# Optimization experiments

Hardware: AMD Instinct MI355X
Metric: run time of the kernel (lower is better)

The kernel has to match this reference:

```python
import jax, jax.numpy as jnp
import numpy as np

B, S, D = 2, 2048, 1024
E, K = 8, 2
I = 938  # expert intermediate: _find_multiple(round(4*1024*2/3),256)//3 = 2816//3


def setup_inputs() -> dict:
    key = jax.random.key(0)
    ks = jax.random.split(key, 6)
    inv_sqrt_d = 1.0 / np.sqrt(D)
    inv_sqrt_i = 1.0 / np.sqrt(I)
    return {
        "hidden_states": jax.random.normal(ks[0], (B, S, D), jnp.float32),
        "gate_weight": jax.random.normal(ks[1], (E, D), jnp.float32) * inv_sqrt_d,
        "shared_gate_up": jax.random.normal(ks[2], (D, 2 * I), jnp.float32) * inv_sqrt_d,
        "shared_down": jax.random.normal(ks[3], (I, D), jnp.float32) * inv_sqrt_i,
        "expert_gate_up": jax.random.normal(ks[4], (E, D, 2 * I), jnp.float32) * inv_sqrt_d,
        "expert_down": jax.random.normal(ks[5], (E, I, D), jnp.float32) * inv_sqrt_i,
    }


def _swiglu(gu, w_down):
    gate, up = jnp.split(gu, 2, axis=-1)
    return (jax.nn.silu(gate) * up) @ w_down


def reference(hidden_states, gate_weight, shared_gate_up, shared_down,
              expert_gate_up, expert_down):
    b, s, d = hidden_states.shape
    x = hidden_states.reshape(-1, d)            # [T, D]
    T = x.shape[0]
    n_experts = gate_weight.shape[0]

    # shared expert (always active)
    out = _swiglu(x @ shared_gate_up, shared_down)

    # router: softmax in fp32, top-k, renormalize
    logits = x @ gate_weight.T                   # [T, E]
    probs = jax.nn.softmax(logits.astype(jnp.float32), axis=-1).astype(x.dtype)
    top_p, top_i = jax.lax.top_k(probs, K)       # [T, K]
    top_p = top_p / (top_p.sum(axis=-1, keepdims=True) + 1e-8)

    # dense combine weights: combine[t, e] = sum_k top_p[t,k] * [top_i[t,k]==e]
    combine = jnp.zeros((T, n_experts), x.dtype).at[
        jnp.arange(T)[:, None], top_i].add(top_p)

    # same math as per-token gathered bmm: sum_e combine[:,e] * expert_e(x)
    for e in range(n_experts):
        out = out + combine[:, e:e + 1] * _swiglu(x @ expert_gate_up[e], expert_down[e])

    return out.reshape(b, s, d)
```

## Files before the change

### kernel.cpp

```cpp
#include <hip/hip_runtime.h>
#include <hip/hip_bf16.h>
#include <stdint.h>

#define T_TOK 4096
#define D_DIM 1024
#define E_EXP 8
#define I_DIM 938
#define TWO_I 1876
#define NP2 2048
#define IP 1024

typedef __attribute__((ext_vector_type(8))) short bf16x8;
typedef __attribute__((ext_vector_type(4))) float f32x4;
typedef __attribute__((ext_vector_type(8))) unsigned short u16x8;
typedef __attribute__((ext_vector_type(4))) unsigned short u16x4;

static __device__ __forceinline__ unsigned short f2bf(float f) {
  union { float f; uint32_t u; } v; v.f = f;
  uint32_t r = v.u + 0x7fffu + ((v.u >> 16) & 1u);
  return (unsigned short)(r >> 16);
}
static __device__ __forceinline__ void gload16(const void* g, void* l) {
  __builtin_amdgcn_global_load_lds((__attribute__((address_space(1))) void*)g,
                                   (__attribute__((address_space(3))) void*)l, 16, 0, 0);
}

__global__ __launch_bounds__(256) void cvt_x_kernel(const float* __restrict__ x,
                                                    unsigned short* __restrict__ xb) {
  int i = blockIdx.x * 256 + threadIdx.x;
  float4 v = reinterpret_cast<const float4*>(x)[i];
  u16x4 o;
  o[0] = f2bf(v.x); o[1] = f2bf(v.y); o[2] = f2bf(v.z); o[3] = f2bf(v.w);
  reinterpret_cast<u16x4*>(xb)[i] = o;
}

__global__ __launch_bounds__(256) void router_kernel(const float* __restrict__ x,
                                                     const float* __restrict__ gw,
                                                     int* __restrict__ ti,
                                                     float* __restrict__ tw) {
  int t = blockIdx.x * 4 + (threadIdx.x >> 6);
  int lane = threadIdx.x & 63;
  const float* xp = x + (size_t)t * D_DIM;
  float xv[16];
  #pragma unroll
  for (int i = 0; i < 16; ++i) xv[i] = xp[lane + i * 64];
  float logit[E_EXP];
  #pragma unroll
  for (int e = 0; e < E_EXP; ++e) {
    const float* wp = gw + (size_t)e * D_DIM;
    float s = 0.f;
    #pragma unroll
    for (int i = 0; i < 16; ++i) s += xv[i] * wp[lane + i * 64];
    #pragma unroll
    for (int o = 32; o; o >>= 1) s += __shfl_xor(s, o);
    logit[e] = s;
  }
  float mx = logit[0];
  #pragma unroll
  for (int e = 1; e < E_EXP; ++e) mx = fmaxf(mx, logit[e]);
  float p[E_EXP], sum = 0.f;
  #pragma unroll
  for (int e = 0; e < E_EXP; ++e) { p[e] = __expf(logit[e] - mx); sum += p[e]; }
  int i1 = 0; float p1 = p[0];
  #pragma unroll
  for (int e = 1; e < E_EXP; ++e) if (p[e] > p1) { p1 = p[e]; i1 = e; }
  int i2 = -1; float p2 = -1.f;
  #pragma unroll
  for (int e = 0; e < E_EXP; ++e) if (e != i1 && p[e] > p2) { p2 = p[e]; i2 = e; }
  float P1 = p1 / sum, P2 = p2 / sum;
  float denom = P1 + P2 + 1e-8f;
  if (lane == 0) {
    ti[2 * t] = i1; ti[2 * t + 1] = i2;
    tw[2 * t] = P1 / denom; tw[2 * t + 1] = P2 / denom;
  }
}

__global__ void zero_cnt_kernel(int* cnt) { if (threadIdx.x < E_EXP) cnt[threadIdx.x] = 0; }

__global__ __launch_bounds__(256) void assign_kernel(const int* __restrict__ ti,
                                                     const float* __restrict__ tw,
                                                     int* __restrict__ cnt,
                                                     int* __restrict__ list,
                                                     float* __restrict__ wl, int cap) {
  int t = blockIdx.x * 256 + threadIdx.x;
  #pragma unroll
  for (int j = 0; j < 2; ++j) {
    int e = ti[2 * t + j];
    float w = tw[2 * t + j];
    int slot = atomicAdd(&cnt[e], 1);
    if (slot < cap) { list[e * cap + slot] = t; wl[e * cap + slot] = w; }
  }
}

__global__ __launch_bounds__(256) void transpose_gu_kernel(
    const float* __restrict__ sgu, const float* __restrict__ egu,
    unsigned short* __restrict__ wT) {
  int e = blockIdx.z;
  const float* w = (e == 0) ? sgu : egu + (size_t)(e - 1) * D_DIM * TWO_I;
  unsigned short* o = wT + (size_t)e * NP2 * D_DIM;
  int k0 = blockIdx.x * 64, n0 = blockIdx.y * 32;
  __shared__ unsigned short lds[32][72];
  int tid = threadIdx.x;
  int nn = tid & 31, kr = tid >> 5;
  int n = n0 + nn;
  int src = (n < IP) ? ((n < I_DIM) ? n : -1)
                     : ((n - IP < I_DIM) ? I_DIM + (n - IP) : -1);
  #pragma unroll
  for (int i = 0; i < 8; ++i) {
    int k = k0 + kr + i * 8;
    float f = (src >= 0) ? w[(size_t)k * TWO_I + src] : 0.f;
    lds[nn][kr + i * 8] = f2bf(f);
  }
  __syncthreads();
  int nr = tid >> 3, kc = (tid & 7) * 8;
  u16x8 v;
  #pragma unroll
  for (int j = 0; j < 8; ++j) v[j] = lds[nr][kc + j];
  *reinterpret_cast<u16x8*>(&o[(size_t)(n0 + nr) * D_DIM + k0 + kc]) = v;
}

__global__ __launch_bounds__(256) void transpose_d_kernel(
    const float* __restrict__ sdn, const float* __restrict__ edn,
    unsigned short* __restrict__ wT) {
  int e = blockIdx.z;
  const float* w = (e == 0) ? sdn : edn + (size_t)(e - 1) * I_DIM * D_DIM;
  unsigned short* o = wT + (size_t)e * D_DIM * IP;
  int k0 = blockIdx.x * 64, n0 = blockIdx.y * 32;
  __shared__ unsigned short lds[32][72];
  int tid = threadIdx.x;
  int nn = tid & 31, kr = tid >> 5;
  #pragma unroll
  for (int i = 0; i < 8; ++i) {
    int k = k0 + kr + i * 8;
    float f = (k < I_DIM) ? w[(size_t)k * D_DIM + n0 + nn] : 0.f;
    lds[nn][kr + i * 8] = f2bf(f);
  }
  __syncthreads();
  int nr = tid >> 3, kc = (tid & 7) * 8;
  u16x8 v;
  #pragma unroll
  for (int j = 0; j < 8; ++j) v[j] = lds[nr][kc + j];
  *reinterpret_cast<u16x8*>(&o[(size_t)(n0 + nr) * IP + k0 + kc]) = v;
}

template<bool GATHER>
__global__ __launch_bounds__(256) void gemm1_kernel(
    const unsigned short* __restrict__ xb,
    const unsigned short* __restrict__ wbase,
    unsigned short* __restrict__ hbase,
    const int* __restrict__ list, const int* __restrict__ cnt, int cap) {
  const int e = blockIdx.z;
  const int m0 = blockIdx.x * 128, n0 = blockIdx.y * 128;
  int count = T_TOK;
  if (GATHER) { count = min(cnt[e], cap); if (m0 >= count) return; }
  const unsigned short* w = wbase + (GATHER ? (size_t)(e + 1) * NP2 * D_DIM : 0);
  unsigned short* h = hbase + (GATHER ? (size_t)e * cap * IP : 0);

  __shared__ __align__(16) unsigned short a_lds[128 * 32];
  __shared__ __align__(16) unsigned short b_lds[256 * 32];
  const int tid = threadIdx.x;
  const int wave = tid >> 6, lane = tid & 63;
  const int mw = (wave >> 1) * 64, nw = (wave & 1) * 64;
  const int fr = lane & 15, fq = lane >> 4;

  const int ko = (tid & 3) * 8;
  int arow[2];
  #pragma unroll
  for (int r = 0; r < 2; ++r) {
    int lr = (tid >> 2) + 64 * r;
    int trow = m0 + lr;
    if (GATHER) trow = list[e * cap + min(trow, count - 1)];
    arow[r] = trow;
  }
  size_t brow[4];
  #pragma unroll
  for (int r = 0; r < 4; ++r) {
    int lr = (tid >> 2) + 64 * r;
    int grow = (lr < 128) ? (n0 + lr) : (IP + n0 + lr - 128);
    brow[r] = (size_t)grow * D_DIM;
  }

  f32x4 accg[4][4], accu[4][4];
  #pragma unroll
  for (int m = 0; m < 4; ++m)
    #pragma unroll
    for (int n = 0; n < 4; ++n) { accg[m][n] = (f32x4)0.f; accu[m][n] = (f32x4)0.f; }

  for (int k0 = 0; k0 < D_DIM; k0 += 32) {
    __syncthreads();
    #pragma unroll
    for (int r = 0; r < 2; ++r)
      gload16(xb + (size_t)arow[r] * D_DIM + k0 + ko, &a_lds[((tid >> 2) + 64 * r) * 32 + ko]);
    #pragma unroll
    for (int r = 0; r < 4; ++r)
      gload16(w + brow[r] + k0 + ko, &b_lds[((tid >> 2) + 64 * r) * 32 + ko]);
    __syncthreads();
    bf16x8 av[4], bg[4], bu[4];
    #pragma unroll
    for (int m = 0; m < 4; ++m)
      av[m] = *reinterpret_cast<const bf16x8*>(&a_lds[(mw + m * 16 + fr) * 32 + fq * 8]);
    #pragma unroll
    for (int n = 0; n < 4; ++n) {
      bg[n] = *reinterpret_cast<const bf16x8*>(&b_lds[(nw + n * 16 + fr) * 32 + fq * 8]);
      bu[n] = *reinterpret_cast<const bf16x8*>(&b_lds[(128 + nw + n * 16 + fr) * 32 + fq * 8]);
    }
    #pragma unroll
    for (int m = 0; m < 4; ++m)
      #pragma unroll
      for (int n = 0; n < 4; ++n) {
        accg[m][n] = __builtin_amdgcn_mfma_f32_16x16x32_bf16(av[m], bg[n], accg[m][n], 0, 0, 0);
        accu[m][n] = __builtin_amdgcn_mfma_f32_16x16x32_bf16(av[m], bu[n], accu[m][n], 0, 0, 0);
      }
  }
  #pragma unroll
  for (int m = 0; m < 4; ++m)
    #pragma unroll
    for (int q = 0; q < 4; ++q) {
      int t = m0 + mw + m * 16 + fq * 4 + q;
      #pragma unroll
      for (int n = 0; n < 4; ++n) {
        float g = accg[m][n][q], u = accu[m][n][q];
        float hv = (g / (1.f + __expf(-g))) * u;
        h[(size_t)t * IP + n0 + nw + n * 16 + fr] = f2bf(hv);
      }
    }
}

template<bool GATHER>
__global__ __launch_bounds__(256) void gemm2_kernel(
    const unsigned short* __restrict__ hbase,
    const unsigned short* __restrict__ wbase,
    float* __restrict__ out,
    const int* __restrict__ list, const float* __restrict__ wl,
    const int* __restrict__ cnt, int cap) {
  const int e = blockIdx.z;
  const int m0 = blockIdx.x * 128, n0 = blockIdx.y * 128;
  int count = T_TOK;
  if (GATHER) { count = min(cnt[e], cap); if (m0 >= count) return; }
  const unsigned short* A = hbase + (GATHER ? (size_t)e * cap * IP : 0);
  const unsigned short* B = wbase + (GATHER ? (size_t)(e + 1) * D_DIM * IP : 0);

  __shared__ __align__(16) unsigned short a_lds[128 * 32];
  __shared__ __align__(16) unsigned short b_lds[128 * 32];
  const int tid = threadIdx.x;
  const int wave = tid >> 6, lane = tid & 63;
  const int mw = (wave >> 1) * 64, nw = (wave & 1) * 64;
  const int fr = lane & 15, fq = lane >> 4;
  const int ko = (tid & 3) * 8;

  f32x4 acc[4][4];
  #pragma unroll
  for (int m = 0; m < 4; ++m)
    #pragma unroll
    for (int n = 0; n < 4; ++n) acc[m][n] = (f32x4)0.f;

  for (int k0 = 0; k0 < IP; k0 += 32) {
    __syncthreads();
    #pragma unroll
    for (int r = 0; r < 2; ++r) {
      int lr = (tid >> 2) + 64 * r;
      gload16(A + (size_t)(m0 + lr) * IP + k0 + ko, &a_lds[lr * 32 + ko]);
      gload16(B + (size_t)(n0 + lr) * IP + k0 + ko, &b_lds[lr * 32 + ko]);
    }
    __syncthreads();
    bf16x8 av[4], bv[4];
    #pragma unroll
    for (int m = 0; m < 4; ++m)
      av[m] = *reinterpret_cast<const bf16x8*>(&a_lds[(mw + m * 16 + fr) * 32 + fq * 8]);
    #pragma unroll
    for (int n = 0; n < 4; ++n)
      bv[n] = *reinterpret_cast<const bf16x8*>(&b_lds[(nw + n * 16 + fr) * 32 + fq * 8]);
    #pragma unroll
    for (int m = 0; m < 4; ++m)
      #pragma unroll
      for (int n = 0; n < 4; ++n)
        acc[m][n] = __builtin_amdgcn_mfma_f32_16x16x32_bf16(av[m], bv[n], acc[m][n], 0, 0, 0);
  }
  #pragma unroll
  for (int m = 0; m < 4; ++m)
    #pragma unroll
    for (int q = 0; q < 4; ++q) {
      int slot = m0 + mw + m * 16 + fq * 4 + q;
      if (GATHER) {
        if (slot < count) {
          int t = list[e * cap + slot];
          float wgt = wl[e * cap + slot];
          #pragma unroll
          for (int n = 0; n < 4; ++n)
            atomicAdd(&out[(size_t)t * D_DIM + n0 + nw + n * 16 + fr], wgt * acc[m][n][q]);
        }
      } else {
        #pragma unroll
        for (int n = 0; n < 4; ++n)
          out[(size_t)slot * D_DIM + n0 + nw + n * 16 + fr] = acc[m][n][q];
      }
    }
}

extern "C" void kernel_launch(void* const* d_in, const int* in_sizes, int n_in,
                              void* d_out, int out_size, void* d_ws, size_t ws_size,
                              hipStream_t stream) {
  const float* x   = (const float*)d_in[0];
  const float* gw  = (const float*)d_in[1];
  const float* sgu = (const float*)d_in[2];
  const float* sdn = (const float*)d_in[3];
  const float* egu = (const float*)d_in[4];
  const float* edn = (const float*)d_in[5];
  float* out = (float*)d_out;

  char* p = (char*)d_ws;
  unsigned short* xb = (unsigned short*)p;  p += (size_t)T_TOK * D_DIM * 2;
  unsigned short* wTgu = (unsigned short*)p; p += (size_t)9 * NP2 * D_DIM * 2;
  unsigned short* wTd  = (unsigned short*)p; p += (size_t)9 * D_DIM * IP * 2;
  size_t fixed_tail = (size_t)T_TOK * 2 * (4 + 4) + 64 + 256;
  size_t used = (size_t)(p - (char*)d_ws) + fixed_tail;
  size_t per_cap = (size_t)E_EXP * (IP * 2 + 4 + 4);
  long avail = (long)ws_size - (long)used;
  int cap = (int)(avail > 0 ? avail / (long)per_cap : 0);
  cap &= ~127;
  if (cap > 2048) cap = 2048;
  if (cap < 1280) cap = 1280;
  if ((size_t)E_EXP * cap * IP < (size_t)T_TOK * IP) cap = 1280;

  unsigned short* h_g = (unsigned short*)p; p += (size_t)E_EXP * cap * IP * 2;
  int*   ti   = (int*)p;   p += (size_t)T_TOK * 2 * 4;
  float* tw   = (float*)p; p += (size_t)T_TOK * 2 * 4;
  int*   list = (int*)p;   p += (size_t)E_EXP * cap * 4;
  float* wl   = (float*)p; p += (size_t)E_EXP * cap * 4;
  int*   cnt  = (int*)p;

  cvt_x_kernel<<<(T_TOK * D_DIM) / (4 * 256), 256, 0, stream>>>(x, xb);
  router_kernel<<<T_TOK / 4, 256, 0, stream>>>(x, gw, ti, tw);
  zero_cnt_kernel<<<1, 64, 0, stream>>>(cnt);
  assign_kernel<<<T_TOK / 256, 256, 0, stream>>>(ti, tw, cnt, list, wl, cap);
  transpose_gu_kernel<<<dim3(D_DIM / 64, NP2 / 32, 9), 256, 0, stream>>>(sgu, egu, wTgu);
  transpose_d_kernel<<<dim3(IP / 64, D_DIM / 32, 9), 256, 0, stream>>>(sdn, edn, wTd);

  gemm1_kernel<false><<<dim3(T_TOK / 128, IP / 128, 1), 256, 0, stream>>>(
      xb, wTgu, h_g, nullptr, nullptr, cap);
  gemm2_kernel<false><<<dim3(T_TOK / 128, D_DIM / 128, 1), 256, 0, stream>>>(
      h_g, wTd, out, nullptr, nullptr, nullptr, cap);
  gemm1_kernel<true><<<dim3(cap / 128, IP / 128, E_EXP), 256, 0, stream>>>(
      xb, wTgu, h_g, list, cnt, cap);
  gemm2_kernel<true><<<dim3(cap / 128, D_DIM / 128, E_EXP), 256, 0, stream>>>(
      h_g, wTd, out, list, wl, cnt, cap);
}
```

Measured before the change: 481.1 us.

## Double-buffer GEMM LDS tiles, merge shared/routed gemm1 launch, remap blocks across XCDs

The GEMM main loops now use two LDS buffers. The next k-tile's global-to-LDS loads are issued before the current tile's MFMAs, with one barrier per iteration instead of two, so load latency can overlap compute. The shared-expert and routed-expert gate/up GEMMs run in a single flattened launch, and the shared expert writes to its own intermediate buffer. Block indices are remapped so that consecutive tiles spread across the chiplet groups. The cost is double the LDS per block, which can lower occupancy, and the routed grids are now sized for a fixed capacity rather than the computed cap.

```diff
diff --git a/kernel.cpp b/kernel.cpp
--- a/kernel.cpp
+++ b/kernel.cpp
@@ -143,39 +143,47 @@
   *reinterpret_cast<u16x8*>(&o[(size_t)(n0 + nr) * IP + k0 + kc]) = v;
 }
 
-template<bool GATHER>
 __global__ __launch_bounds__(256) void gemm1_kernel(
     const unsigned short* __restrict__ xb,
-    const unsigned short* __restrict__ wbase,
-    unsigned short* __restrict__ hbase,
+    const unsigned short* __restrict__ wTgu,
+    unsigned short* __restrict__ h_sh,
+    unsigned short* __restrict__ h_g,
     const int* __restrict__ list, const int* __restrict__ cnt, int cap) {
-  const int e = blockIdx.z;
-  const int m0 = blockIdx.x * 128, n0 = blockIdx.y * 128;
+  const int orig = blockIdx.x;
+  const int wg = (orig & 7) * (gridDim.x >> 3) + (orig >> 3);
+  const int e = wg >> 8;
+  const int rem = wg & 255;
+  const int m0 = (rem >> 3) * 128, n0 = (rem & 7) * 128;
   int count = T_TOK;
-  if (GATHER) { count = min(cnt[e], cap); if (m0 >= count) return; }
-  const unsigned short* w = wbase + (GATHER ? (size_t)(e + 1) * NP2 * D_DIM : 0);
-  unsigned short* h = hbase + (GATHER ? (size_t)e * cap * IP : 0);
-
-  __shared__ __align__(16) unsigned short a_lds[128 * 32];
-  __shared__ __align__(16) unsigned short b_lds[256 * 32];
+  const unsigned short* w = wTgu;
+  unsigned short* h = h_sh;
+  if (e > 0) {
+    count = min(cnt[e - 1], cap);
+    if (m0 >= count) return;
+    w = wTgu + (size_t)e * NP2 * D_DIM;
+    h = h_g + (size_t)(e - 1) * cap * IP;
+  }
+
+  __shared__ __align__(16) unsigned short a_lds[2][128 * 32];
+  __shared__ __align__(16) unsigned short b_lds[2][256 * 32];
   const int tid = threadIdx.x;
   const int wave = tid >> 6, lane = tid & 63;
   const int mw = (wave >> 1) * 64, nw = (wave & 1) * 64;
   const int fr = lane & 15, fq = lane >> 4;
-
   const int ko = (tid & 3) * 8;
-  int arow[2];
+  const int ldr = tid >> 2;
+
+  size_t arow[2];
   #pragma unroll
   for (int r = 0; r < 2; ++r) {
-    int lr = (tid >> 2) + 64 * r;
-    int trow = m0 + lr;
-    if (GATHER) trow = list[e * cap + min(trow, count - 1)];
-    arow[r] = trow;
+    int trow = m0 + ldr + 64 * r;
+    if (e > 0) trow = list[(e - 1) * cap + min(trow, count - 1)];
+    arow[r] = (size_t)trow * D_DIM;
   }
   size_t brow[4];
   #pragma unroll
   for (int r = 0; r < 4; ++r) {
-    int lr = (tid >> 2) + 64 * r;
+    int lr = ldr + 64 * r;
     int grow = (lr < 128) ? (n0 + lr) : (IP + n0 + lr - 128);
     brow[r] = (size_t)grow * D_DIM;
   }
@@ -186,23 +194,28 @@
     #pragma unroll
     for (int n = 0; n < 4; ++n) { accg[m][n] = (f32x4)0.f; accu[m][n] = (f32x4)0.f; }
 
-  for (int k0 = 0; k0 < D_DIM; k0 += 32) {
-    __syncthreads();
+  auto stage = [&](int buf, int k0) {
     #pragma unroll
     for (int r = 0; r < 2; ++r)
-      gload16(xb + (size_t)arow[r] * D_DIM + k0 + ko, &a_lds[((tid >> 2) + 64 * r) * 32 + ko]);
+      gload16(xb + arow[r] + k0 + ko, &a_lds[buf][(ldr + 64 * r) * 32 + ko]);
     #pragma unroll
     for (int r = 0; r < 4; ++r)
-      gload16(w + brow[r] + k0 + ko, &b_lds[((tid >> 2) + 64 * r) * 32 + ko]);
-    __syncthreads();
+      gload16(w + brow[r] + k0 + ko, &b_lds[buf][(ldr + 64 * r) * 32 + ko]);
+  };
+
+  stage(0, 0);
+  __syncthreads();
+  int cur = 0;
+  for (int t = 0; t < D_DIM / 32; ++t) {
+    if (t + 1 < D_DIM / 32) stage(cur ^ 1, (t + 1) * 32);
     bf16x8 av[4], bg[4], bu[4];
     #pragma unroll
     for (int m = 0; m < 4; ++m)
-      av[m] = *reinterpret_cast<const bf16x8*>(&a_lds[(mw + m * 16 + fr) * 32 + fq * 8]);
+      av[m] = *reinterpret_cast<const bf16x8*>(&a_lds[cur][(mw + m * 16 + fr) * 32 + fq * 8]);
     #pragma unroll
     for (int n = 0; n < 4; ++n) {
-      bg[n] = *reinterpret_cast<const bf16x8*>(&b_lds[(nw + n * 16 + fr) * 32 + fq * 8]);
-      bu[n] = *reinterpret_cast<const bf16x8*>(&b_lds[(128 + nw + n * 16 + fr) * 32 + fq * 8]);
+      bg[n] = *reinterpret_cast<const bf16x8*>(&b_lds[cur][(nw + n * 16 + fr) * 32 + fq * 8]);
+      bu[n] = *reinterpret_cast<const bf16x8*>(&b_lds[cur][(128 + nw + n * 16 + fr) * 32 + fq * 8]);
     }
     #pragma unroll
     for (int m = 0; m < 4; ++m)
@@ -211,6 +224,8 @@
         accg[m][n] = __builtin_amdgcn_mfma_f32_16x16x32_bf16(av[m], bg[n], accg[m][n], 0, 0, 0);
         accu[m][n] = __builtin_amdgcn_mfma_f32_16x16x32_bf16(av[m], bu[n], accu[m][n], 0, 0, 0);
       }
+    __syncthreads();
+    cur ^= 1;
   }
   #pragma unroll
   for (int m = 0; m < 4; ++m)
@@ -226,27 +241,19 @@
     }
 }
 
-template<bool GATHER>
-__global__ __launch_bounds__(256) void gemm2_kernel(
-    const unsigned short* __restrict__ hbase,
-    const unsigned short* __restrict__ wbase,
-    float* __restrict__ out,
-    const int* __restrict__ list, const float* __restrict__ wl,
-    const int* __restrict__ cnt, int cap) {
-  const int e = blockIdx.z;
+__global__ __launch_bounds__(256) void gemm2_sh_kernel(
+    const unsigned short* __restrict__ A,
+    const unsigned short* __restrict__ B,
+    float* __restrict__ out) {
   const int m0 = blockIdx.x * 128, n0 = blockIdx.y * 128;
-  int count = T_TOK;
-  if (GATHER) { count = min(cnt[e], cap); if (m0 >= count) return; }
-  const unsigned short* A = hbase + (GATHER ? (size_t)e * cap * IP : 0);
-  const unsigned short* B = wbase + (GATHER ? (size_t)(e + 1) * D_DIM * IP : 0);
-
-  __shared__ __align__(16) unsigned short a_lds[128 * 32];
-  __shared__ __align__(16) unsigned short b_lds[128 * 32];
+  __shared__ __align__(16) unsigned short a_lds[2][128 * 32];
+  __shared__ __align__(16) unsigned short b_lds[2][128 * 32];
   const int tid = threadIdx.x;
   const int wave = tid >> 6, lane = tid & 63;
   const int mw = (wave >> 1) * 64, nw = (wave & 1) * 64;
   const int fr = lane & 15, fq = lane >> 4;
   const int ko = (tid & 3) * 8;
+  const int ldr = tid >> 2;
 
   f32x4 acc[4][4];
   #pragma unroll
@@ -254,45 +261,115 @@
     #pragma unroll
     for (int n = 0; n < 4; ++n) acc[m][n] = (f32x4)0.f;
 
-  for (int k0 = 0; k0 < IP; k0 += 32) {
-    __syncthreads();
+  auto stage = [&](int buf, int k0) {
     #pragma unroll
     for (int r = 0; r < 2; ++r) {
-      int lr = (tid >> 2) + 64 * r;
-      gload16(A + (size_t)(m0 + lr) * IP + k0 + ko, &a_lds[lr * 32 + ko]);
-      gload16(B + (size_t)(n0 + lr) * IP + k0 + ko, &b_lds[lr * 32 + ko]);
-    }
-    __syncthreads();
+      int lr = ldr + 64 * r;
+      gload16(A + (size_t)(m0 + lr) * IP + k0 + ko, &a_lds[buf][lr * 32 + ko]);
+      gload16(B + (size_t)(n0 + lr) * IP + k0 + ko, &b_lds[buf][lr * 32 + ko]);
+    }
+  };
+  stage(0, 0);
+  __syncthreads();
+  int cur = 0;
+  for (int t = 0; t < IP / 32; ++t) {
+    if (t + 1 < IP / 32) stage(cur ^ 1, (t + 1) * 32);
     bf16x8 av[4], bv[4];
     #pragma unroll
     for (int m = 0; m < 4; ++m)
-      av[m] = *reinterpret_cast<const bf16x8*>(&a_lds[(mw + m * 16 + fr) * 32 + fq * 8]);
+      av[m] = *reinterpret_cast<const bf16x8*>(&a_lds[cur][(mw + m * 16 + fr) * 32 + fq * 8]);
     #pragma unroll
     for (int n = 0; n < 4; ++n)
-      bv[n] = *reinterpret_cast<const bf16x8*>(&b_lds[(nw + n * 16 + fr) * 32 + fq * 8]);
+      bv[n] = *reinterpret_cast<const bf16x8*>(&b_lds[cur][(nw + n * 16 + fr) * 32 + fq * 8]);
     #pragma unroll
     for (int m = 0; m < 4; ++m)
       #pragma unroll
       for (int n = 0; n < 4; ++n)
         acc[m][n] = __builtin_amdgcn_mfma_f32_16x16x32_bf16(av[m], bv[n], acc[m][n], 0, 0, 0);
+    __syncthreads();
+    cur ^= 1;
+  }
+  #pragma unroll
+  for (int m = 0; m < 4; ++m)
+    #pragma unroll
+    for (int q = 0; q < 4; ++q) {
+      int t = m0 + mw + m * 16 + fq * 4 + q;
+      #pragma unroll
+      for (int n = 0; n < 4; ++n)
+        out[(size_t)t * D_DIM + n0 + nw + n * 16 + fr] = acc[m][n][q];
+    }
+}
+
+__global__ __launch_bounds__(256) void gemm2_rt_kernel(
+    const unsigned short* __restrict__ h_g,
+    const unsigned short* __restrict__ wTd,
+    float* __restrict__ out,
+    const int* __restrict__ list, const float* __restrict__ wl,
+    const int* __restrict__ cnt, int cap) {
+  const int orig = blockIdx.x;
+  const int wg = (orig & 7) * (gridDim.x >> 3) + (orig >> 3);
+  const int e = wg >> 7;
+  const int rem = wg & 127;
+  const int m0 = (rem >> 3) * 128, n0 = (rem & 7) * 128;
+  const int count = min(cnt[e], cap);
+  if (m0 >= count) return;
+  const unsigned short* A = h_g + (size_t)e * cap * IP;
+  const unsigned short* B = wTd + (size_t)(e + 1) * D_DIM * IP;
+
+  __shared__ __align__(16) unsigned short a_lds[2][128 * 32];
+  __shared__ __align__(16) unsigned short b_lds[2][128 * 32];
+  const int tid = threadIdx.x;
+  const int wave = tid >> 6, lane = tid & 63;
+  const int mw = (wave >> 1) * 64, nw = (wave & 1) * 64;
+  const int fr = lane & 15, fq = lane >> 4;
+  const int ko = (tid & 3) * 8;
+  const int ldr = tid >> 2;
+
+  f32x4 acc[4][4];
+  #pragma unroll
+  for (int m = 0; m < 4; ++m)
+    #pragma unroll
+    for (int n = 0; n < 4; ++n) acc[m][n] = (f32x4)0.f;
+
+  auto stage = [&](int buf, int k0) {
+    #pragma unroll
+    for (int r = 0; r < 2; ++r) {
+      int lr = ldr + 64 * r;
+      gload16(A + (size_t)(m0 + lr) * IP + k0 + ko, &a_lds[buf][lr * 32 + ko]);
+      gload16(B + (size_t)(n0 + lr) * IP + k0 + ko, &b_lds[buf][lr * 32 + ko]);
+    }
+  };
+  stage(0, 0);
+  __syncthreads();
+  int cur = 0;
+  for (int t = 0; t < IP / 32; ++t) {
+    if (t + 1 < IP / 32) stage(cur ^ 1, (t + 1) * 32);
+    bf16x8 av[4], bv[4];
+    #pragma unroll
+    for (int m = 0; m < 4; ++m)
+      av[m] = *reinterpret_cast<const bf16x8*>(&a_lds[cur][(mw + m * 16 + fr) * 32 + fq * 8]);
+    #pragma unroll
+    for (int n = 0; n < 4; ++n)
+      bv[n] = *reinterpret_cast<const bf16x8*>(&b_lds[cur][(nw + n * 16 + fr) * 32 + fq * 8]);
+    #pragma unroll
+    for (int m = 0; m < 4; ++m)
+      #pragma unroll
+      for (int n = 0; n < 4; ++n)
+        acc[m][n] = __builtin_amdgcn_mfma_f32_16x16x32_bf16(av[m], bv[n], acc[m][n], 0, 0, 0);
+    __syncthreads();
+    cur ^= 1;
   }
   #pragma unroll
   for (int m = 0; m < 4; ++m)
     #pragma unroll
     for (int q = 0; q < 4; ++q) {
       int slot = m0 + mw + m * 16 + fq * 4 + q;
-      if (GATHER) {
-        if (slot < count) {
-          int t = list[e * cap + slot];
-          float wgt = wl[e * cap + slot];
-          #pragma unroll
-          for (int n = 0; n < 4; ++n)
-            atomicAdd(&out[(size_t)t * D_DIM + n0 + nw + n * 16 + fr], wgt * acc[m][n][q]);
-        }
-      } else {
+      if (slot < count) {
+        int t = list[e * cap + slot];
+        float wgt = wl[e * cap + slot];
         #pragma unroll
         for (int n = 0; n < 4; ++n)
-          out[(size_t)slot * D_DIM + n0 + nw + n * 16 + fr] = acc[m][n][q];
+          atomicAdd(&out[(size_t)t * D_DIM + n0 + nw + n * 16 + fr], wgt * acc[m][n][q]);
       }
     }
 }
@@ -309,9 +386,11 @@
   float* out = (float*)d_out;
 
   char* p = (char*)d_ws;
-  unsigned short* xb = (unsigned short*)p;  p += (size_t)T_TOK * D_DIM * 2;
+  unsigned short* xb   = (unsigned short*)p; p += (size_t)T_TOK * D_DIM * 2;
   unsigned short* wTgu = (unsigned short*)p; p += (size_t)9 * NP2 * D_DIM * 2;
   unsigned short* wTd  = (unsigned short*)p; p += (size_t)9 * D_DIM * IP * 2;
+  unsigned short* h_sh = (unsigned short*)p; p += (size_t)T_TOK * IP * 2;
+
   size_t fixed_tail = (size_t)T_TOK * 2 * (4 + 4) + 64 + 256;
   size_t used = (size_t)(p - (char*)d_ws) + fixed_tail;
   size_t per_cap = (size_t)E_EXP * (IP * 2 + 4 + 4);
@@ -320,7 +399,6 @@
   cap &= ~127;
   if (cap > 2048) cap = 2048;
   if (cap < 1280) cap = 1280;
-  if ((size_t)E_EXP * cap * IP < (size_t)T_TOK * IP) cap = 1280;
 
   unsigned short* h_g = (unsigned short*)p; p += (size_t)E_EXP * cap * IP * 2;
   int*   ti   = (int*)p;   p += (size_t)T_TOK * 2 * 4;
@@ -336,12 +414,7 @@
   transpose_gu_kernel<<<dim3(D_DIM / 64, NP2 / 32, 9), 256, 0, stream>>>(sgu, egu, wTgu);
   transpose_d_kernel<<<dim3(IP / 64, D_DIM / 32, 9), 256, 0, stream>>>(sdn, edn, wTd);
 
-  gemm1_kernel<false><<<dim3(T_TOK / 128, IP / 128, 1), 256, 0, stream>>>(
-      xb, wTgu, h_g, nullptr, nullptr, cap);
-  gemm2_kernel<false><<<dim3(T_TOK / 128, D_DIM / 128, 1), 256, 0, stream>>>(
-      h_g, wTd, out, nullptr, nullptr, nullptr, cap);
-  gemm1_kernel<true><<<dim3(cap / 128, IP / 128, E_EXP), 256, 0, stream>>>(
-      xb, wTgu, h_g, list, cnt, cap);
-  gemm2_kernel<true><<<dim3(cap / 128, D_DIM / 128, E_EXP), 256, 0, stream>>>(
-      h_g, wTd, out, list, wl, cnt, cap);
-}
+  gemm1_kernel<<<9 * 32 * 8, 256, 0, stream>>>(xb, wTgu, h_sh, h_g, list, cnt, cap);
+  gemm2_sh_kernel<<<dim3(T_TOK / 128, D_DIM / 128), 256, 0, stream>>>(h_sh, wTd, out);
+  gemm2_rt_kernel<<<8 * 16 * 8, 256, 0, stream>>>(h_g, wTd, out, list, wl, cnt, cap);
+}
```

Measured after the change: 489.1 us. Within noise of the previous version (+1.7%).

## Merge shared and routed expert GEMMs into single launches with 256x256 tiles

Applied to the files above, without the earlier changes.

Interleaves gate and up columns in the transposed gate_up weights so one accumulator tile holds both, and pairs them with a lane shuffle in the epilogue. GEMM tiles grow to 256x256 with K=64 per stage and 512 threads. The shared and routed expert work for each GEMM now runs in one launch with an XCD-aware block remap, and output is zeroed with a memset so the shared expert also accumulates atomically. This cuts launches and raises data reuse per tile, at the cost of higher register and LDS pressure, lower occupancy, and extra atomic traffic for the shared expert output.

```diff
diff --git a/kernel.cpp b/kernel.cpp
--- a/kernel.cpp
+++ b/kernel.cpp
@@ -103,8 +103,8 @@
   int tid = threadIdx.x;
   int nn = tid & 31, kr = tid >> 5;
   int n = n0 + nn;
-  int src = (n < IP) ? ((n < I_DIM) ? n : -1)
-                     : ((n - IP < I_DIM) ? I_DIM + (n - IP) : -1);
+  int hc = n >> 1;
+  int src = (hc < I_DIM) ? ((n & 1) ? (I_DIM + hc) : hc) : -1;
   #pragma unroll
   for (int i = 0; i < 8; ++i) {
     int k = k0 + kr + i * 8;
@@ -143,156 +143,167 @@
   *reinterpret_cast<u16x8*>(&o[(size_t)(n0 + nr) * IP + k0 + kc]) = v;
 }
 
-template<bool GATHER>
-__global__ __launch_bounds__(256) void gemm1_kernel(
+__global__ __launch_bounds__(512) void gemm1_kernel(
     const unsigned short* __restrict__ xb,
-    const unsigned short* __restrict__ wbase,
-    unsigned short* __restrict__ hbase,
+    const unsigned short* __restrict__ wTgu,
+    unsigned short* __restrict__ h_sh,
+    unsigned short* __restrict__ h_g,
     const int* __restrict__ list, const int* __restrict__ cnt, int cap) {
-  const int e = blockIdx.z;
-  const int m0 = blockIdx.x * 128, n0 = blockIdx.y * 128;
+  const int orig = blockIdx.x;
+  const int wg = (orig & 7) * (gridDim.x >> 3) + (orig >> 3);
+  int e, mb, nb;
+  if (wg < 128) { e = 0; mb = wg >> 3; nb = wg & 7; }
+  else { int r = wg - 128; e = 1 + (r >> 6); int rem = r & 63; mb = rem >> 3; nb = rem & 7; }
+  const int m0 = mb * 256, n0 = nb * 256;
   int count = T_TOK;
-  if (GATHER) { count = min(cnt[e], cap); if (m0 >= count) return; }
-  const unsigned short* w = wbase + (GATHER ? (size_t)(e + 1) * NP2 * D_DIM : 0);
-  unsigned short* h = hbase + (GATHER ? (size_t)e * cap * IP : 0);
-
-  __shared__ __align__(16) unsigned short a_lds[128 * 32];
-  __shared__ __align__(16) unsigned short b_lds[256 * 32];
+  unsigned short* h = h_sh;
+  if (e > 0) {
+    count = min(cnt[e - 1], cap);
+    if (m0 >= count) return;
+    h = h_g + (size_t)(e - 1) * cap * IP;
+  }
+  const unsigned short* w = wTgu + (size_t)e * NP2 * D_DIM;
+
+  __shared__ __align__(16) unsigned short a_lds[256 * 64];
+  __shared__ __align__(16) unsigned short b_lds[256 * 64];
   const int tid = threadIdx.x;
   const int wave = tid >> 6, lane = tid & 63;
-  const int mw = (wave >> 1) * 64, nw = (wave & 1) * 64;
+  const int mw = (wave >> 2) * 128, nw = (wave & 3) * 64;
   const int fr = lane & 15, fq = lane >> 4;
-
-  const int ko = (tid & 3) * 8;
-  int arow[2];
-  #pragma unroll
-  for (int r = 0; r < 2; ++r) {
-    int lr = (tid >> 2) + 64 * r;
-    int trow = m0 + lr;
-    if (GATHER) trow = list[e * cap + min(trow, count - 1)];
-    arow[r] = trow;
-  }
-  size_t brow[4];
-  #pragma unroll
-  for (int r = 0; r < 4; ++r) {
-    int lr = (tid >> 2) + 64 * r;
-    int grow = (lr < 128) ? (n0 + lr) : (IP + n0 + lr - 128);
-    brow[r] = (size_t)grow * D_DIM;
-  }
-
-  f32x4 accg[4][4], accu[4][4];
-  #pragma unroll
-  for (int m = 0; m < 4; ++m)
-    #pragma unroll
-    for (int n = 0; n < 4; ++n) { accg[m][n] = (f32x4)0.f; accu[m][n] = (f32x4)0.f; }
-
-  for (int k0 = 0; k0 < D_DIM; k0 += 32) {
+  const int srow = tid >> 3;
+  const int sk = (tid & 7) * 8;
+
+  size_t arow[4], brow[4];
+  #pragma unroll
+  for (int c = 0; c < 4; ++c) {
+    int rr = m0 + 64 * c + srow;
+    if (e > 0) rr = list[(e - 1) * cap + min(rr, count - 1)];
+    arow[c] = (size_t)rr * D_DIM;
+    brow[c] = (size_t)(n0 + 64 * c + srow) * D_DIM;
+  }
+
+  f32x4 acc[8][4];
+  #pragma unroll
+  for (int m = 0; m < 8; ++m)
+    #pragma unroll
+    for (int n = 0; n < 4; ++n) acc[m][n] = (f32x4)0.f;
+
+  for (int k0 = 0; k0 < D_DIM; k0 += 64) {
     __syncthreads();
     #pragma unroll
-    for (int r = 0; r < 2; ++r)
-      gload16(xb + (size_t)arow[r] * D_DIM + k0 + ko, &a_lds[((tid >> 2) + 64 * r) * 32 + ko]);
-    #pragma unroll
-    for (int r = 0; r < 4; ++r)
-      gload16(w + brow[r] + k0 + ko, &b_lds[((tid >> 2) + 64 * r) * 32 + ko]);
+    for (int c = 0; c < 4; ++c) {
+      gload16(xb + arow[c] + k0 + sk, &a_lds[(64 * c + srow) * 64 + sk]);
+      gload16(w + brow[c] + k0 + sk, &b_lds[(64 * c + srow) * 64 + sk]);
+    }
     __syncthreads();
-    bf16x8 av[4], bg[4], bu[4];
-    #pragma unroll
-    for (int m = 0; m < 4; ++m)
-      av[m] = *reinterpret_cast<const bf16x8*>(&a_lds[(mw + m * 16 + fr) * 32 + fq * 8]);
-    #pragma unroll
-    for (int n = 0; n < 4; ++n) {
-      bg[n] = *reinterpret_cast<const bf16x8*>(&b_lds[(nw + n * 16 + fr) * 32 + fq * 8]);
-      bu[n] = *reinterpret_cast<const bf16x8*>(&b_lds[(128 + nw + n * 16 + fr) * 32 + fq * 8]);
-    }
-    #pragma unroll
-    for (int m = 0; m < 4; ++m)
-      #pragma unroll
-      for (int n = 0; n < 4; ++n) {
-        accg[m][n] = __builtin_amdgcn_mfma_f32_16x16x32_bf16(av[m], bg[n], accg[m][n], 0, 0, 0);
-        accu[m][n] = __builtin_amdgcn_mfma_f32_16x16x32_bf16(av[m], bu[n], accu[m][n], 0, 0, 0);
+    #pragma unroll
+    for (int kk = 0; kk < 2; ++kk) {
+      bf16x8 av[8], bv[4];
+      #pragma unroll
+      for (int m = 0; m < 8; ++m)
+        av[m] = *reinterpret_cast<const bf16x8*>(&a_lds[(mw + m * 16 + fr) * 64 + kk * 32 + fq * 8]);
+      #pragma unroll
+      for (int n = 0; n < 4; ++n)
+        bv[n] = *reinterpret_cast<const bf16x8*>(&b_lds[(nw + n * 16 + fr) * 64 + kk * 32 + fq * 8]);
+      #pragma unroll
+      for (int m = 0; m < 8; ++m)
+        #pragma unroll
+        for (int n = 0; n < 4; ++n)
+          acc[m][n] = __builtin_amdgcn_mfma_f32_16x16x32_bf16(av[m], bv[n], acc[m][n], 0, 0, 0);
+    }
+  }
+  const bool isGate = !(fr & 1);
+  const int hcb = (n0 + nw) >> 1;
+  #pragma unroll
+  for (int m = 0; m < 8; ++m)
+    #pragma unroll
+    for (int n = 0; n < 4; ++n)
+      #pragma unroll
+      for (int q = 0; q < 4; ++q) {
+        float v = acc[m][n][q];
+        float pt = __shfl_xor(v, 1);
+        if (isGate) {
+          float hv = (v / (1.f + __expf(-v))) * pt;
+          int trow = m0 + mw + m * 16 + fq * 4 + q;
+          h[(size_t)trow * IP + hcb + n * 8 + (fr >> 1)] = f2bf(hv);
+        }
       }
-  }
-  #pragma unroll
-  for (int m = 0; m < 4; ++m)
-    #pragma unroll
-    for (int q = 0; q < 4; ++q) {
-      int t = m0 + mw + m * 16 + fq * 4 + q;
-      #pragma unroll
-      for (int n = 0; n < 4; ++n) {
-        float g = accg[m][n][q], u = accu[m][n][q];
-        float hv = (g / (1.f + __expf(-g))) * u;
-        h[(size_t)t * IP + n0 + nw + n * 16 + fr] = f2bf(hv);
-      }
-    }
-}
-
-template<bool GATHER>
-__global__ __launch_bounds__(256) void gemm2_kernel(
-    const unsigned short* __restrict__ hbase,
-    const unsigned short* __restrict__ wbase,
+}
+
+__global__ __launch_bounds__(512) void gemm2_kernel(
+    const unsigned short* __restrict__ h_sh,
+    const unsigned short* __restrict__ h_g,
+    const unsigned short* __restrict__ wTd,
     float* __restrict__ out,
     const int* __restrict__ list, const float* __restrict__ wl,
     const int* __restrict__ cnt, int cap) {
-  const int e = blockIdx.z;
-  const int m0 = blockIdx.x * 128, n0 = blockIdx.y * 128;
+  const int orig = blockIdx.x;
+  const int wg = (orig & 7) * (gridDim.x >> 3) + (orig >> 3);
+  int e, mb, nb;
+  if (wg < 64) { e = -1; mb = wg >> 2; nb = wg & 3; }
+  else { int r = wg - 64; e = r >> 5; int rem = r & 31; mb = rem >> 2; nb = rem & 3; }
+  const int m0 = mb * 256, n0 = nb * 256;
   int count = T_TOK;
-  if (GATHER) { count = min(cnt[e], cap); if (m0 >= count) return; }
-  const unsigned short* A = hbase + (GATHER ? (size_t)e * cap * IP : 0);
-  const unsigned short* B = wbase + (GATHER ? (size_t)(e + 1) * D_DIM * IP : 0);
-
-  __shared__ __align__(16) unsigned short a_lds[128 * 32];
-  __shared__ __align__(16) unsigned short b_lds[128 * 32];
+  const unsigned short* A = h_sh;
+  if (e >= 0) {
+    count = min(cnt[e], cap);
+    if (m0 >= count) return;
+    A = h_g + (size_t)e * cap * IP;
+  }
+  const unsigned short* B = wTd + (size_t)(e + 1) * D_DIM * IP;
+
+  __shared__ __align__(16) unsigned short a_lds[256 * 64];
+  __shared__ __align__(16) unsigned short b_lds[256 * 64];
   const int tid = threadIdx.x;
   const int wave = tid >> 6, lane = tid & 63;
-  const int mw = (wave >> 1) * 64, nw = (wave & 1) * 64;
+  const int mw = (wave >> 2) * 128, nw = (wave & 3) * 64;
   const int fr = lane & 15, fq = lane >> 4;
-  const int ko = (tid & 3) * 8;
-
-  f32x4 acc[4][4];
-  #pragma unroll
-  for (int m = 0; m < 4; ++m)
+  const int srow = tid >> 3;
+  const int sk = (tid & 7) * 8;
+
+  f32x4 acc[8][4];
+  #pragma unroll
+  for (int m = 0; m < 8; ++m)
     #pragma unroll
     for (int n = 0; n < 4; ++n) acc[m][n] = (f32x4)0.f;
 
-  for (int k0 = 0; k0 < IP; k0 += 32) {
+  for (int k0 = 0; k0 < IP; k0 += 64) {
     __syncthreads();
     #pragma unroll
-    for (int r = 0; r < 2; ++r) {
-      int lr = (tid >> 2) + 64 * r;
-      gload16(A + (size_t)(m0 + lr) * IP + k0 + ko, &a_lds[lr * 32 + ko]);
-      gload16(B + (size_t)(n0 + lr) * IP + k0 + ko, &b_lds[lr * 32 + ko]);
+    for (int c = 0; c < 4; ++c) {
+      gload16(A + (size_t)(m0 + 64 * c + srow) * IP + k0 + sk,
+              &a_lds[(64 * c + srow) * 64 + sk]);
+      gload16(B + (size_t)(n0 + 64 * c + srow) * IP + k0 + sk,
+              &b_lds[(64 * c + srow) * 64 + sk]);
     }
     __syncthreads();
-    bf16x8 av[4], bv[4];
-    #pragma unroll
-    for (int m = 0; m < 4; ++m)
-      av[m] = *reinterpret_cast<const bf16x8*>(&a_lds[(mw + m * 16 + fr) * 32 + fq * 8]);
-    #pragma unroll
-    for (int n = 0; n < 4; ++n)
-      bv[n] = *reinterpret_cast<const bf16x8*>(&b_lds[(nw + n * 16 + fr) * 32 + fq * 8]);
-    #pragma unroll
-    for (int m = 0; m < 4; ++m)
+    #pragma unroll
+    for (int kk = 0; kk < 2; ++kk) {
+      bf16x8 av[8], bv[4];
+      #pragma unroll
+      for (int m = 0; m < 8; ++m)
+        av[m] = *reinterpret_cast<const bf16x8*>(&a_lds[(mw + m * 16 + fr) * 64 + kk * 32 + fq * 8]);
       #pragma unroll
       for (int n = 0; n < 4; ++n)
-        acc[m][n] = __builtin_amdgcn_mfma_f32_16x16x32_bf16(av[m], bv[n], acc[m][n], 0, 0, 0);
-  }
-  #pragma unroll
-  for (int m = 0; m < 4; ++m)
+        bv[n] = *reinterpret_cast<const bf16x8*>(&b_lds[(nw + n * 16 + fr) * 64 + kk * 32 + fq * 8]);
+      #pragma unroll
+      for (int m = 0; m < 8; ++m)
+        #pragma unroll
+        for (int n = 0; n < 4; ++n)
+          acc[m][n] = __builtin_amdgcn_mfma_f32_16x16x32_bf16(av[m], bv[n], acc[m][n], 0, 0, 0);
+    }
+  }
+  #pragma unroll
+  for (int m = 0; m < 8; ++m)
     #pragma unroll
     for (int q = 0; q < 4; ++q) {
       int slot = m0 + mw + m * 16 + fq * 4 + q;
-      if (GATHER) {
-        if (slot < count) {
-          int t = list[e * cap + slot];
-          float wgt = wl[e * cap + slot];
-          #pragma unroll
-          for (int n = 0; n < 4; ++n)
-            atomicAdd(&out[(size_t)t * D_DIM + n0 + nw + n * 16 + fr], wgt * acc[m][n][q]);
-        }
-      } else {
+      if (slot < count) {
+        int t = slot; float wgt = 1.f;
+        if (e >= 0) { t = list[e * cap + slot]; wgt = wl[e * cap + slot]; }
         #pragma unroll
         for (int n = 0; n < 4; ++n)
-          out[(size_t)slot * D_DIM + n0 + nw + n * 16 + fr] = acc[m][n][q];
+          atomicAdd(&out[(size_t)t * D_DIM + n0 + nw + n * 16 + fr], wgt * acc[m][n][q]);
       }
     }
 }
@@ -309,18 +320,19 @@
   float* out = (float*)d_out;
 
   char* p = (char*)d_ws;
-  unsigned short* xb = (unsigned short*)p;  p += (size_t)T_TOK * D_DIM * 2;
+  unsigned short* xb   = (unsigned short*)p; p += (size_t)T_TOK * D_DIM * 2;
   unsigned short* wTgu = (unsigned short*)p; p += (size_t)9 * NP2 * D_DIM * 2;
   unsigned short* wTd  = (unsigned short*)p; p += (size_t)9 * D_DIM * IP * 2;
+  unsigned short* h_sh = (unsigned short*)p; p += (size_t)T_TOK * IP * 2;
+
   size_t fixed_tail = (size_t)T_TOK * 2 * (4 + 4) + 64 + 256;
   size_t used = (size_t)(p - (char*)d_ws) + fixed_tail;
   size_t per_cap = (size_t)E_EXP * (IP * 2 + 4 + 4);
   long avail = (long)ws_size - (long)used;
   int cap = (int)(avail > 0 ? avail / (long)per_cap : 0);
-  cap &= ~127;
+  cap &= ~255;
   if (cap > 2048) cap = 2048;
-  if (cap < 1280) cap = 1280;
-  if ((size_t)E_EXP * cap * IP < (size_t)T_TOK * IP) cap = 1280;
+  if (cap < 1536) cap = 1536;
 
   unsigned short* h_g = (unsigned short*)p; p += (size_t)E_EXP * cap * IP * 2;
   int*   ti   = (int*)p;   p += (size_t)T_TOK * 2 * 4;
@@ -335,13 +347,8 @@
   assign_kernel<<<T_TOK / 256, 256, 0, stream>>>(ti, tw, cnt, list, wl, cap);
   transpose_gu_kernel<<<dim3(D_DIM / 64, NP2 / 32, 9), 256, 0, stream>>>(sgu, egu, wTgu);
   transpose_d_kernel<<<dim3(IP / 64, D_DIM / 32, 9), 256, 0, stream>>>(sdn, edn, wTd);
-
-  gemm1_kernel<false><<<dim3(T_TOK / 128, IP / 128, 1), 256, 0, stream>>>(
-      xb, wTgu, h_g, nullptr, nullptr, cap);
-  gemm2_kernel<false><<<dim3(T_TOK / 128, D_DIM / 128, 1), 256, 0, stream>>>(
-      h_g, wTd, out, nullptr, nullptr, nullptr, cap);
-  gemm1_kernel<true><<<dim3(cap / 128, IP / 128, E_EXP), 256, 0, stream>>>(
-      xb, wTgu, h_g, list, cnt, cap);
-  gemm2_kernel<true><<<dim3(cap / 128, D_DIM / 128, E_EXP), 256, 0, stream>>>(
-      h_g, wTd, out, list, wl, cnt, cap);
-}
+  hipMemsetAsync(d_out, 0, (size_t)out_size * 4, stream);
+
+  gemm1_kernel<<<128 + E_EXP * 64, 512, 0, stream>>>(xb, wTgu, h_sh, h_g, list, cnt, cap);
+  gemm2_kernel<<<64 + E_EXP * 32, 512, 0, stream>>>(h_sh, h_g, wTd, out, list, wl, cnt, cap);
+}
```

Measured after the change: 505.2 us. 1.05x slower.
